# Performance work log

Measured on AMD Instinct MI355X. Metric: run time of the kernel, lower is better.

The kernel has to match this reference:

```python
import jax, jax.numpy as jnp
import numpy as np

K_CENTERS = 10
G_CENTERS = 2
EPS = 1e-12  # tf.math.l2_normalize epsilon


def setup_inputs() -> dict:
    key = jax.random.key(0)
    k1, k2, k3 = jax.random.split(key, 3)
    B, H, W, D = 16, 16, 64, 512
    KC = K_CENTERS + G_CENTERS
    feat = jax.random.normal(k1, (B, H, W, D), dtype=jnp.float32)
    cluster_score = jax.random.normal(k2, (B, H, W, KC), dtype=jnp.float32)
    cluster = jax.random.normal(k3, (KC, D), dtype=jnp.float32)
    return {"feat": feat, "cluster_score": cluster_score, "cluster": cluster}


def reference(feat, cluster_score, cluster):
    B, H, W, D = feat.shape
    KC = cluster.shape[0]
    # Softmax over clusters (stable)
    A = jax.nn.softmax(cluster_score, axis=-1)            # [B,H,W,KC]
    # Flatten spatial dims: sum_{s} A[b,s,k] * (feat[b,s,d] - cluster[k,d])
    Af = A.reshape(B, H * W, KC)
    ff = feat.reshape(B, H * W, D)
    # = einsum(A, feat) - (sum_s A)[b,k] * cluster[k,d]  (avoids [B,S,KC,D] intermediate)
    cluster_res = jnp.einsum('bsk,bsd->bkd', Af, ff) - Af.sum(axis=1)[..., None] * cluster[None]
    # GhostVLAD: keep only real clusters
    cluster_res = cluster_res[:, :K_CENTERS, :]           # [B,K,D]
    # L2 normalize over feature dim
    sq = jnp.sum(cluster_res * cluster_res, axis=-1, keepdims=True)
    cluster_l2 = cluster_res * jax.lax.rsqrt(jnp.maximum(sq, EPS))
    return cluster_l2.reshape(B, K_CENTERS * D)
```

## Files before the change

### kernel.cpp

```cpp
#include <hip/hip_runtime.h>


#define B_   16
#define S_   1024
#define D_   512
#define KC_  12
#define K_   10
#define KL_  5
#define NT   512
#define NPAR 4

__global__ __launch_bounds__(NT) void vlad_fused(
    const float* __restrict__ feat, const float* __restrict__ score,
    const float* __restrict__ cluster, float* __restrict__ out)
{
    const int x    = blockIdx.x;
    const int half = (x >> 3) & 1;
    const int b    = (x & 7) | ((x >> 4) << 3);
    const int k0   = half * KL_;

    const int tid  = threadIdx.x;
    const int lane = tid & 63;
    const int wave = tid >> 6;
    const int par  = tid >> 7;
    const int col  = tid & 127;

    __shared__ float  As[S_][8];
    __shared__ float4 red[NPAR - 1][KL_][128];
    __shared__ float  wpart[8][KL_];
    __shared__ float  asumL[KL_];
    __shared__ float  wsumL[2][KL_];

    float aw[KL_];
    #pragma unroll
    for (int j = 0; j < KL_; j++) aw[j] = 0.f;

    #pragma unroll
    for (int t = 0; t < 2; t++) {
        const int s = tid + t * NT;
        const float4* sp = (const float4*)(score + (size_t)(b * S_ + s) * KC_);
        const float4 w0 = sp[0], w1 = sp[1], w2 = sp[2];
        float xv[KC_] = {w0.x, w0.y, w0.z, w0.w, w1.x, w1.y, w1.z, w1.w,
                         w2.x, w2.y, w2.z, w2.w};
        float m = xv[0];
        #pragma unroll
        for (int k = 1; k < KC_; k++) m = fmaxf(m, xv[k]);
        float sum = 0.f;
        #pragma unroll
        for (int k = 0; k < KC_; k++) { xv[k] = __expf(xv[k] - m); sum += xv[k]; }
        const float inv = 1.0f / sum;
        const float a0 = xv[k0] * inv, a1 = xv[k0 + 1] * inv,
                    a2 = xv[k0 + 2] * inv, a3 = xv[k0 + 3] * inv,
                    a4 = xv[k0 + 4] * inv;
        *(float4*)&As[s][0] = make_float4(a0, a1, a2, a3);
        As[s][4] = a4;
        aw[0] += a0; aw[1] += a1; aw[2] += a2; aw[3] += a3; aw[4] += a4;
    }
    #pragma unroll
    for (int j = 0; j < KL_; j++) {
        float r = aw[j];
        #pragma unroll
        for (int off = 32; off > 0; off >>= 1) r += __shfl_down(r, off, 64);
        if (lane == 0) wpart[wave][j] = r;
    }
    __syncthreads();
    if (tid < KL_) {
        float s = 0.f;
        #pragma unroll
        for (int w = 0; w < 8; w++) s += wpart[w][tid];
        asumL[tid] = s;
    }

    float acc[KL_][4];
    #pragma unroll
    for (int k = 0; k < KL_; k++)
        acc[k][0] = acc[k][1] = acc[k][2] = acc[k][3] = 0.f;

    const float4* fp = (const float4*)(feat + (size_t)b * S_ * D_) + col;
    #pragma unroll 8
    for (int i = 0; i < S_ / NPAR; i++) {
        const int s = (i << 2) | par;
        const float4 v   = fp[(size_t)s * (D_ / 4)];
        const float4 a03 = *(const float4*)&As[s][0];
        const float  a4  = As[s][4];
        acc[0][0] += a03.x * v.x; acc[0][1] += a03.x * v.y;
        acc[0][2] += a03.x * v.z; acc[0][3] += a03.x * v.w;
        acc[1][0] += a03.y * v.x; acc[1][1] += a03.y * v.y;
        acc[1][2] += a03.y * v.z; acc[1][3] += a03.y * v.w;
        acc[2][0] += a03.z * v.x; acc[2][1] += a03.z * v.y;
        acc[2][2] += a03.z * v.z; acc[2][3] += a03.z * v.w;
        acc[3][0] += a03.w * v.x; acc[3][1] += a03.w * v.y;
        acc[3][2] += a03.w * v.z; acc[3][3] += a03.w * v.w;
        acc[4][0] += a4   * v.x; acc[4][1] += a4   * v.y;
        acc[4][2] += a4   * v.z; acc[4][3] += a4   * v.w;
    }

    if (par) {
        #pragma unroll
        for (int k = 0; k < KL_; k++)
            red[par - 1][k][col] =
                make_float4(acc[k][0], acc[k][1], acc[k][2], acc[k][3]);
    }
    __syncthreads();

    float r[KL_][4];
    float sq[KL_];
    if (!par) {
        #pragma unroll
        for (int k = 0; k < KL_; k++) {
            float v0 = acc[k][0], v1 = acc[k][1], v2 = acc[k][2], v3 = acc[k][3];
            #pragma unroll
            for (int p = 0; p < NPAR - 1; p++) {
                const float4 t = red[p][k][col];
                v0 += t.x; v1 += t.y; v2 += t.z; v3 += t.w;
            }
            const float  asv = asumL[k];
            const float4 cv  = *(const float4*)(cluster + (size_t)(k0 + k) * D_ + col * 4);
            v0 -= asv * cv.x; v1 -= asv * cv.y; v2 -= asv * cv.z; v3 -= asv * cv.w;
            r[k][0] = v0; r[k][1] = v1; r[k][2] = v2; r[k][3] = v3;
            sq[k] = v0 * v0 + v1 * v1 + v2 * v2 + v3 * v3;
        }
        #pragma unroll
        for (int k = 0; k < KL_; k++) {
            float s = sq[k];
            #pragma unroll
            for (int off = 32; off > 0; off >>= 1) s += __shfl_down(s, off, 64);
            if (lane == 0) wsumL[wave][k] = s;
        }
    }
    __syncthreads();

    if (!par) {
        #pragma unroll
        for (int k = 0; k < KL_; k++) {
            const float tot = wsumL[0][k] + wsumL[1][k];
            const float sc  = rsqrtf(fmaxf(tot, 1e-12f));
            *(float4*)(out + (size_t)(b * K_ + k0 + k) * D_ + col * 4) =
                make_float4(r[k][0] * sc, r[k][1] * sc, r[k][2] * sc, r[k][3] * sc);
        }
    }
}

extern "C" void kernel_launch(void* const* d_in, const int* in_sizes, int n_in,
                              void* d_out, int out_size, void* d_ws, size_t ws_size,
                              hipStream_t stream) {
    const float* feat    = (const float*)d_in[0];
    const float* score   = (const float*)d_in[1];
    const float* cluster = (const float*)d_in[2];
    float* out = (float*)d_out;
    (void)d_ws; (void)ws_size;

    vlad_fused<<<B_ * 2, NT, 0, stream>>>(feat, score, cluster, out);
}
```

Before: 93.87 us.

## Split work to one block per batch and cluster, with contiguous spatial chunks

The grid grows from 32 blocks (batch x half of the clusters) to 160 blocks (batch x single cluster), so more CUs on the GPU are used. Each of the four thread groups now walks a contiguous quarter of the spatial rows instead of interleaved rows, and reads four assignment weights per LDS float4 load. The cost is that every block rereads the full feature slab for its batch and recomputes the softmax, giving roughly 5x more global reads, which are expected to hit in L2/MALL. The block-to-XCD mapping keeps blocks of the same batch on the same XCD so those rereads can share cache.

```diff
diff --git a/kernel.cpp b/kernel.cpp
--- a/kernel.cpp
+++ b/kernel.cpp
@@ -6,138 +6,104 @@
 #define D_   512
 #define KC_  12
 #define K_   10
-#define KL_  5
 #define NT   512
-#define NPAR 4
 
 __global__ __launch_bounds__(NT) void vlad_fused(
     const float* __restrict__ feat, const float* __restrict__ score,
     const float* __restrict__ cluster, float* __restrict__ out)
 {
-    const int x    = blockIdx.x;
-    const int half = (x >> 3) & 1;
-    const int b    = (x & 7) | ((x >> 4) << 3);
-    const int k0   = half * KL_;
+    const int bid = blockIdx.x;
+    const int xcd = bid & 7;
+    const int j   = bid >> 3;
+    const int b   = xcd * 2 + (j / K_);
+    const int k   = j % K_;
 
     const int tid  = threadIdx.x;
+    const int col  = tid & 127;
+    const int par  = tid >> 7;
     const int lane = tid & 63;
     const int wave = tid >> 6;
-    const int par  = tid >> 7;
-    const int col  = tid & 127;
 
-    __shared__ float  As[S_][8];
-    __shared__ float4 red[NPAR - 1][KL_][128];
-    __shared__ float  wpart[8][KL_];
-    __shared__ float  asumL[KL_];
-    __shared__ float  wsumL[2][KL_];
+    __shared__ __align__(16) float As[S_];
+    __shared__ float  wred[8];
+    __shared__ float  asumS;
+    __shared__ float4 red[3][128];
+    __shared__ float  wsum[2];
 
-    float aw[KL_];
-    #pragma unroll
-    for (int j = 0; j < KL_; j++) aw[j] = 0.f;
+    float4 cv = make_float4(0.f, 0.f, 0.f, 0.f);
+    if (tid < 128)
+        cv = ((const float4*)(cluster + (size_t)k * D_))[col];
 
+    float aw = 0.f;
     #pragma unroll
     for (int t = 0; t < 2; t++) {
         const int s = tid + t * NT;
-        const float4* sp = (const float4*)(score + (size_t)(b * S_ + s) * KC_);
-        const float4 w0 = sp[0], w1 = sp[1], w2 = sp[2];
-        float xv[KC_] = {w0.x, w0.y, w0.z, w0.w, w1.x, w1.y, w1.z, w1.w,
-                         w2.x, w2.y, w2.z, w2.w};
-        float m = xv[0];
-        #pragma unroll
-        for (int k = 1; k < KC_; k++) m = fmaxf(m, xv[k]);
-        float sum = 0.f;
-        #pragma unroll
-        for (int k = 0; k < KC_; k++) { xv[k] = __expf(xv[k] - m); sum += xv[k]; }
-        const float inv = 1.0f / sum;
-        const float a0 = xv[k0] * inv, a1 = xv[k0 + 1] * inv,
-                    a2 = xv[k0 + 2] * inv, a3 = xv[k0 + 3] * inv,
-                    a4 = xv[k0 + 4] * inv;
-        *(float4*)&As[s][0] = make_float4(a0, a1, a2, a3);
-        As[s][4] = a4;
-        aw[0] += a0; aw[1] += a1; aw[2] += a2; aw[3] += a3; aw[4] += a4;
+        const float* srow = score + (size_t)(b * S_ + s) * KC_;
+        const float4 w0 = ((const float4*)srow)[0];
+        const float4 w1 = ((const float4*)srow)[1];
+        const float4 w2 = ((const float4*)srow)[2];
+        const float  xk = srow[k];
+        float m = fmaxf(fmaxf(fmaxf(w0.x, w0.y), fmaxf(w0.z, w0.w)),
+                 fmaxf(fmaxf(fmaxf(w1.x, w1.y), fmaxf(w1.z, w1.w)),
+                       fmaxf(fmaxf(w2.x, w2.y), fmaxf(w2.z, w2.w))));
+        float sum = __expf(w0.x - m) + __expf(w0.y - m) + __expf(w0.z - m) +
+                    __expf(w0.w - m) + __expf(w1.x - m) + __expf(w1.y - m) +
+                    __expf(w1.z - m) + __expf(w1.w - m) + __expf(w2.x - m) +
+                    __expf(w2.y - m) + __expf(w2.z - m) + __expf(w2.w - m);
+        const float a = __expf(xk - m) / sum;
+        As[s] = a;
+        aw += a;
     }
     #pragma unroll
-    for (int j = 0; j < KL_; j++) {
-        float r = aw[j];
+    for (int off = 32; off > 0; off >>= 1) aw += __shfl_down(aw, off, 64);
+    if (lane == 0) wred[wave] = aw;
+    __syncthreads();
+    if (tid == 0) {
+        float s = 0.f;
         #pragma unroll
-        for (int off = 32; off > 0; off >>= 1) r += __shfl_down(r, off, 64);
-        if (lane == 0) wpart[wave][j] = r;
+        for (int w = 0; w < 8; w++) s += wred[w];
+        asumS = s;
+    }
+
+    const float4* fp  = (const float4*)(feat + (size_t)(b * S_ + par * 256) * D_) + col;
+    const float4* As4 = (const float4*)&As[par * 256];
+    float4 acc = make_float4(0.f, 0.f, 0.f, 0.f);
+    #pragma unroll 8
+    for (int i4 = 0; i4 < 64; i4++) {
+        const float4 a4 = As4[i4];
+        const float4 v0 = fp[(size_t)(i4 * 4 + 0) * 128];
+        const float4 v1 = fp[(size_t)(i4 * 4 + 1) * 128];
+        const float4 v2 = fp[(size_t)(i4 * 4 + 2) * 128];
+        const float4 v3 = fp[(size_t)(i4 * 4 + 3) * 128];
+        acc.x += a4.x * v0.x + a4.y * v1.x + a4.z * v2.x + a4.w * v3.x;
+        acc.y += a4.x * v0.y + a4.y * v1.y + a4.z * v2.y + a4.w * v3.y;
+        acc.z += a4.x * v0.z + a4.y * v1.z + a4.z * v2.z + a4.w * v3.z;
+        acc.w += a4.x * v0.w + a4.y * v1.w + a4.z * v2.w + a4.w * v3.w;
+    }
+
+    if (par) red[par - 1][col] = acc;
+    __syncthreads();
+
+    float4 r;
+    float  sq = 0.f;
+    if (!par) {
+        const float4 r0 = red[0][col], r1 = red[1][col], r2 = red[2][col];
+        const float asv = asumS;
+        r.x = acc.x + r0.x + r1.x + r2.x - asv * cv.x;
+        r.y = acc.y + r0.y + r1.y + r2.y - asv * cv.y;
+        r.z = acc.z + r0.z + r1.z + r2.z - asv * cv.z;
+        r.w = acc.w + r0.w + r1.w + r2.w - asv * cv.w;
+        sq = r.x * r.x + r.y * r.y + r.z * r.z + r.w * r.w;
+        #pragma unroll
+        for (int off = 32; off > 0; off >>= 1) sq += __shfl_down(sq, off, 64);
+        if (lane == 0) wsum[wave] = sq;
     }
     __syncthreads();
-    if (tid < KL_) {
-        float s = 0.f;
-        #pragma unroll
-        for (int w = 0; w < 8; w++) s += wpart[w][tid];
-        asumL[tid] = s;
-    }
-
-    float acc[KL_][4];
-    #pragma unroll
-    for (int k = 0; k < KL_; k++)
-        acc[k][0] = acc[k][1] = acc[k][2] = acc[k][3] = 0.f;
-
-    const float4* fp = (const float4*)(feat + (size_t)b * S_ * D_) + col;
-    #pragma unroll 8
-    for (int i = 0; i < S_ / NPAR; i++) {
-        const int s = (i << 2) | par;
-        const float4 v   = fp[(size_t)s * (D_ / 4)];
-        const float4 a03 = *(const float4*)&As[s][0];
-        const float  a4  = As[s][4];
-        acc[0][0] += a03.x * v.x; acc[0][1] += a03.x * v.y;
-        acc[0][2] += a03.x * v.z; acc[0][3] += a03.x * v.w;
-        acc[1][0] += a03.y * v.x; acc[1][1] += a03.y * v.y;
-        acc[1][2] += a03.y * v.z; acc[1][3] += a03.y * v.w;
-        acc[2][0] += a03.z * v.x; acc[2][1] += a03.z * v.y;
-        acc[2][2] += a03.z * v.z; acc[2][3] += a03.z * v.w;
-        acc[3][0] += a03.w * v.x; acc[3][1] += a03.w * v.y;
-        acc[3][2] += a03.w * v.z; acc[3][3] += a03.w * v.w;
-        acc[4][0] += a4   * v.x; acc[4][1] += a4   * v.y;
-        acc[4][2] += a4   * v.z; acc[4][3] += a4   * v.w;
-    }
-
-    if (par) {
-        #pragma unroll
-        for (int k = 0; k < KL_; k++)
-            red[par - 1][k][col] =
-                make_float4(acc[k][0], acc[k][1], acc[k][2], acc[k][3]);
-    }
-    __syncthreads();
-
-    float r[KL_][4];
-    float sq[KL_];
     if (!par) {
-        #pragma unroll
-        for (int k = 0; k < KL_; k++) {
-            float v0 = acc[k][0], v1 = acc[k][1], v2 = acc[k][2], v3 = acc[k][3];
-            #pragma unroll
-            for (int p = 0; p < NPAR - 1; p++) {
-                const float4 t = red[p][k][col];
-                v0 += t.x; v1 += t.y; v2 += t.z; v3 += t.w;
-            }
-            const float  asv = asumL[k];
-            const float4 cv  = *(const float4*)(cluster + (size_t)(k0 + k) * D_ + col * 4);
-            v0 -= asv * cv.x; v1 -= asv * cv.y; v2 -= asv * cv.z; v3 -= asv * cv.w;
-            r[k][0] = v0; r[k][1] = v1; r[k][2] = v2; r[k][3] = v3;
-            sq[k] = v0 * v0 + v1 * v1 + v2 * v2 + v3 * v3;
-        }
-        #pragma unroll
-        for (int k = 0; k < KL_; k++) {
-            float s = sq[k];
-            #pragma unroll
-            for (int off = 32; off > 0; off >>= 1) s += __shfl_down(s, off, 64);
-            if (lane == 0) wsumL[wave][k] = s;
-        }
-    }
-    __syncthreads();
-
-    if (!par) {
-        #pragma unroll
-        for (int k = 0; k < KL_; k++) {
-            const float tot = wsumL[0][k] + wsumL[1][k];
-            const float sc  = rsqrtf(fmaxf(tot, 1e-12f));
-            *(float4*)(out + (size_t)(b * K_ + k0 + k) * D_ + col * 4) =
-                make_float4(r[k][0] * sc, r[k][1] * sc, r[k][2] * sc, r[k][3] * sc);
-        }
+        const float tot   = wsum[0] + wsum[1];
+        const float scale = rsqrtf(fmaxf(tot, 1e-12f));
+        ((float4*)(out + (size_t)(b * K_ + k) * D_))[col] =
+            make_float4(r.x * scale, r.y * scale, r.z * scale, r.w * scale);
     }
 }
 
@@ -150,5 +116,5 @@
     float* out = (float*)d_out;
     (void)d_ws; (void)ws_size;
 
-    vlad_fused<<<B_ * 2, NT, 0, stream>>>(feat, score, cluster, out);
+    vlad_fused<<<B_ * K_, NT, 0, stream>>>(feat, score, cluster, out);
 }
```

Result: no change. 94.72 us (+0.9%).
